# Performance work log

Hardware: AMD Instinct MI355X
Metric: run time of the kernel (lower is better)

## Reference

```python
import jax, jax.numpy as jnp
import numpy as np

BEV = 128          # bev_res
EMBED = 128        # embed_dim
HEADS = 8
POINTS = 4
HD = EMBED // HEADS  # head dim = 16


def setup_inputs() -> dict:
    key = jax.random.key(0)
    ks = jax.random.split(key, 9)
    bs, nq = 4, BEV * BEV
    s = lambda k, shape: jax.random.normal(k, shape, jnp.float32) * 0.02
    return {
        "query": jax.random.normal(ks[0], (bs, nq, EMBED), jnp.float32),
        "W_off": s(ks[1], (EMBED, HEADS * POINTS * 2)),
        "b_off": s(ks[2], (HEADS * POINTS * 2,)),
        "W_attn": s(ks[3], (EMBED, HEADS * POINTS)),
        "b_attn": s(ks[4], (HEADS * POINTS,)),
        "W_val": s(ks[5], (EMBED, EMBED)),
        "b_val": s(ks[6], (EMBED,)),
        "W_out": s(ks[7], (EMBED, EMBED)),
        "b_out": s(ks[8], (EMBED,)),
    }


def _ref_points():
    # matches np.meshgrid(linspace(0,1,BEV), linspace(0,1,BEV), indexing='ij');
    # stacked as (col, row) = (x, y), flattened row-major to (BEV*BEV, 2)
    lin = jnp.linspace(0.0, 1.0, BEV)
    gy, gx = jnp.meshgrid(lin, lin, indexing="ij")
    return jnp.stack([gx, gy], axis=-1).reshape(-1, 2)


def _msda(query, W_off, b_off, W_attn, b_attn, W_val, b_val, W_out, b_out):
    bs, nq, _ = query.shape
    H = W = BEV
    # value projection; single level so num_value == nq == H*W
    value = query @ W_val + b_val
    v = value.reshape(bs, nq, HEADS, HD).transpose(0, 2, 1, 3)  # (bs, heads, HW, hd)

    # sampling offsets and attention weights (softmax over levels*points = points)
    off = (query @ W_off + b_off).reshape(bs, nq, HEADS, POINTS, 2)
    aw = jax.nn.softmax((query @ W_attn + b_attn).reshape(bs, nq, HEADS, POINTS), axis=-1)

    ref = _ref_points()  # (nq, 2) in [0,1], (x, y)
    norm = jnp.array([W, H], jnp.float32)  # offset_normalizer = (W, H)
    loc = ref[None, :, None, None, :] + off / norm  # (bs, nq, heads, pts, 2)

    # grid_sample bilinear, align_corners=False, padding_mode='zeros'
    px = loc[..., 0] * W - 0.5
    py = loc[..., 1] * H - 0.5
    x0 = jnp.floor(px)
    y0 = jnp.floor(py)
    wx = px - x0  # weight toward x0+1
    wy = py - y0
    x0i = x0.astype(jnp.int32)
    y0i = y0.astype(jnp.int32)

    def flat(a):  # (bs, nq, heads, pts) -> (bs, heads, nq*pts)
        return a.transpose(0, 2, 1, 3).reshape(bs, HEADS, nq * POINTS)

    def samp(xi, yi):
        valid = ((xi >= 0) & (xi < W) & (yi >= 0) & (yi < H)).astype(v.dtype)
        xc = jnp.clip(xi, 0, W - 1)
        yc = jnp.clip(yi, 0, H - 1)
        idx = flat(yc * W + xc)  # (bs, heads, nq*pts)
        g = jnp.take_along_axis(v, idx[..., None], axis=2)  # (bs, heads, nq*pts, hd)
        return g * flat(valid)[..., None]

    s00 = samp(x0i, y0i)
    s01 = samp(x0i + 1, y0i)
    s10 = samp(x0i, y0i + 1)
    s11 = samp(x0i + 1, y0i + 1)
    wxf = flat(wx)[..., None]
    wyf = flat(wy)[..., None]
    sampled = (s00 * (1 - wxf) * (1 - wyf) + s01 * wxf * (1 - wyf)
               + s10 * (1 - wxf) * wyf + s11 * wxf * wyf)
    sampled = sampled.reshape(bs, HEADS, nq, POINTS, HD)

    awt = aw.transpose(0, 2, 1, 3)  # (bs, heads, nq, pts)
    out = jnp.einsum("bhnpd,bhnp->bnhd", sampled, awt).reshape(bs, nq, EMBED)
    out = out @ W_out + b_out
    # mmcv MSDA adds identity (=query) internally; SelfAttention adds residual again
    return out + 2.0 * query


def reference(query, W_off, b_off, W_attn, b_attn, W_val, b_val, W_out, b_out):
    return _msda(query, W_off, b_off, W_attn, b_attn, W_val, b_val, W_out, b_out)
```

## Files before the change

### kernel.cpp

```cpp
#include <hip/hip_runtime.h>

#define BS 4
#define NQ 16384

typedef unsigned short u16;
typedef unsigned int u32;
typedef unsigned char u8;
typedef __attribute__((ext_vector_type(8))) short bf16x8;
typedef __attribute__((ext_vector_type(4))) short bf16x4;
typedef __attribute__((ext_vector_type(4))) float f32x4;
typedef __attribute__((ext_vector_type(2))) float f32x2;

__device__ __forceinline__ float bf2f(u16 v) { return __uint_as_float(((u32)v) << 16); }
__device__ __forceinline__ u16 f2bf(float f) {
    u32 u = __float_as_uint(f);
    return (u16)((u + 0x7fffu + ((u >> 16) & 1u)) >> 16);
}
__device__ __forceinline__ u32 pk_trunc(float lo, float hi) {
    return __builtin_amdgcn_perm(__float_as_uint(hi), __float_as_uint(lo), 0x07060302u);
}

union ABu { bf16x8 v; u32 u[4]; };

__global__ __launch_bounds__(256)
void setup_kernel(const float* __restrict__ W_val, const float* __restrict__ W_off,
                  const float* __restrict__ W_attn, const float* __restrict__ W_out,
                  u16* __restrict__ Wswz, u16* __restrict__ Wout_swz)
{
    const int i = blockIdx.x * 256 + threadIdx.x;
    if (i < 28672) {
        const int j = i & 7, lane = (i >> 3) & 15, quad = (i >> 7) & 3;
        const int kb = (i >> 9) & 3, nt = i >> 11;
        const int k = kb * 32 + quad * 8 + j;
        const int n = nt * 16 + lane;
        float v;
        if (n < 128)      v = W_val[k * 128 + n];
        else if (n < 192) v = W_off[k * 64 + (n - 128)];
        else              v = W_attn[k * 32 + (n - 192)];
        Wswz[i] = f2bf(v);
    } else if (i < 45056) {
        const int i2 = i - 28672;
        const int j = i2 & 7, lane = (i2 >> 3) & 15, quad = (i2 >> 7) & 3;
        const int kb = (i2 >> 9) & 3, nt = i2 >> 11;
        const int k = kb * 32 + quad * 8 + j;
        const int n = nt * 16 + lane;
        Wout_swz[i2] = f2bf(W_out[k * 128 + n]);
    }
}

__global__ __launch_bounds__(256, 4)
void fused_kernel(const float* __restrict__ query,
                  const float* __restrict__ b_off, const float* __restrict__ b_attn,
                  const float* __restrict__ b_val, const float* __restrict__ b_out,
                  const u16* __restrict__ Wswz, const u16* __restrict__ Wout_swz,
                  float* __restrict__ out)
{
    __shared__ __align__(16) u8  vhalo[144 * 144];
    __shared__ __align__(16) u16 scratch[64 * 136];

    const int tid = threadIdx.x;
    const int bid = blockIdx.x;
    const int b_  = bid >> 8;
    const int sq  = bid & 255;
    const int Y   = (sq >> 4) * 8;
    const int X   = (sq & 15) * 8;

    const int w = tid >> 6, l = tid & 63;
    const int lane16 = l & 15, quad = l >> 4;
    const size_t batch_base = (size_t)b_ * NQ;

    const bf16x8* Wf  = (const bf16x8*)Wswz;
    const bf16x8* WfO = (const bf16x8*)Wout_swz;

    {
        const int tl = w * 16 + lane16;
        const int ty = tl >> 3, tx = tl & 7;
        const float* qrow = query + (batch_base + (size_t)(Y + ty) * 128 + (X + tx)) * 128
                          + quad * 8;
        bf16x8 qfrag[4];
        #pragma unroll
        for (int kb = 0; kb < 4; ++kb) {
            f32x4 q0 = *(const f32x4*)(qrow + kb * 32);
            f32x4 q1 = *(const f32x4*)(qrow + kb * 32 + 4);
            ABu ab;
            ab.u[0] = pk_trunc(q0.x, q0.y); ab.u[1] = pk_trunc(q0.z, q0.w);
            ab.u[2] = pk_trunc(q1.x, q1.y); ab.u[3] = pk_trunc(q1.z, q1.w);
            qfrag[kb] = ab.v;
        }
        #pragma unroll
        for (int ntile = 0; ntile < 6; ++ntile) {
            const int nt = 8 + ntile;
            f32x4 acc = {0.f, 0.f, 0.f, 0.f};
            const bf16x8* wp = Wf + ((size_t)(nt * 4) * 4 + quad) * 16 + lane16;
            #pragma unroll
            for (int kb = 0; kb < 4; ++kb)
                acc = __builtin_amdgcn_mfma_f32_16x16x32_bf16(wp[kb * 64], qfrag[kb], acc, 0, 0, 0);
            const int c = ntile * 16 + quad * 4;
            const float4 bias = (ntile < 4) ? *(const float4*)&b_off[c]
                                            : *(const float4*)&b_attn[c - 64];
            uint2 pk;
            pk.x = pk_trunc(acc[0] + bias.x, acc[1] + bias.y);
            pk.y = pk_trunc(acc[2] + bias.z, acc[3] + bias.w);
            *(uint2*)&scratch[tl * 96 + c] = pk;
        }
    }

    #pragma unroll
    for (int i = 0; i < 3; ++i) {
        const int a = w + 4 * i;
        if (a >= 9) break;
        const int hp = a * 16 + lane16;
        const int hy = hp / 12, hx = hp - hy * 12;
        const int gy = min(max(Y - 2 + hy, 0), 127);
        const int gx = min(max(X - 2 + hx, 0), 127);
        const float* qrow = query + (batch_base + (size_t)gy * 128 + gx) * 128 + quad * 8;
        bf16x8 qfrag[4];
        #pragma unroll
        for (int kb = 0; kb < 4; ++kb) {
            f32x4 q0 = *(const f32x4*)(qrow + kb * 32);
            f32x4 q1 = *(const f32x4*)(qrow + kb * 32 + 4);
            ABu ab;
            ab.u[0] = pk_trunc(q0.x, q0.y); ab.u[1] = pk_trunc(q0.z, q0.w);
            ab.u[2] = pk_trunc(q1.x, q1.y); ab.u[3] = pk_trunc(q1.z, q1.w);
            qfrag[kb] = ab.v;
        }
        #pragma unroll
        for (int mt = 0; mt < 8; ++mt) {
            f32x4 acc = {0.f, 0.f, 0.f, 0.f};
            const bf16x8* wp = Wf + ((size_t)(mt * 4) * 4 + quad) * 16 + lane16;
            #pragma unroll
            for (int kb = 0; kb < 4; ++kb)
                acc = __builtin_amdgcn_mfma_f32_16x16x32_bf16(wp[kb * 64], qfrag[kb], acc, 0, 0, 0);
            const int d0 = mt * 16 + quad * 4;
            const float4 bias = *(const float4*)&b_val[d0];
            u32 pk = __builtin_amdgcn_cvt_pk_fp8_f32(acc[0] + bias.x, acc[1] + bias.y, 0, false);
            pk     = __builtin_amdgcn_cvt_pk_fp8_f32(acc[2] + bias.z, acc[3] + bias.w, pk, true);
            *(u32*)&vhalo[hp * 144 + d0] = pk;
        }
    }
    __syncthreads();

    float aw[2][4], ox[2][4], oy[2][4];
    #pragma unroll
    for (int it = 0; it < 2; ++it) {
        const int item = it * 256 + tid;
        const int t = item >> 3, h = item & 7;
        bf16x8 ofr = *(const bf16x8*)&scratch[t * 96 + h * 8];
        bf16x4 atr = *(const bf16x4*)&scratch[t * 96 + 64 + h * 4];
        #pragma unroll
        for (int p = 0; p < 4; ++p) {
            ox[it][p] = bf2f((u16)ofr[2 * p]);
            oy[it][p] = bf2f((u16)ofr[2 * p + 1]);
        }
        const float l0 = bf2f((u16)atr[0]), l1 = bf2f((u16)atr[1]);
        const float l2 = bf2f((u16)atr[2]), l3 = bf2f((u16)atr[3]);
        const float m = fmaxf(fmaxf(l0, l1), fmaxf(l2, l3));
        const float e0 = __expf(l0 - m), e1 = __expf(l1 - m);
        const float e2 = __expf(l2 - m), e3 = __expf(l3 - m);
        const float inv = 1.0f / (e0 + e1 + e2 + e3);
        aw[it][0] = e0 * inv; aw[it][1] = e1 * inv;
        aw[it][2] = e2 * inv; aw[it][3] = e3 * inv;
    }
    __syncthreads();

    #pragma unroll
    for (int it = 0; it < 2; ++it) {
        const int item = it * 256 + tid;
        const int t = item >> 3, h = item & 7;
        const int qx = X + (t & 7), qy = Y + (t >> 3);
        const float cx = (float)qx * (128.0f / 127.0f);
        const float cy = (float)qy * (128.0f / 127.0f);

        f32x2 acc2[8];
        #pragma unroll
        for (int d = 0; d < 8; ++d) acc2[d] = (f32x2){0.f, 0.f};

        #pragma unroll
        for (int p = 0; p < 4; ++p) {
            const float px = cx + ox[it][p] - 0.5f;
            const float py = cy + oy[it][p] - 0.5f;
            const float fx = floorf(px), fy = floorf(py);
            const float wx = px - fx, wy = py - fy;
            const int xi = (int)fx, yi = (int)fy;
            const float cw[4] = {(1.f - wx) * (1.f - wy), wx * (1.f - wy),
                                 (1.f - wx) * wy,         wx * wy};
            const int hx0 = min(max(xi - X + 2, 0), 11), hx1 = min(hx0 + 1, 11);
            const int hy0 = min(max(yi - Y + 2, 0), 11), hy1 = min(hy0 + 1, 11);
            const int cxs[4] = {hx0, hx1, hx0, hx1};
            const int cys[4] = {hy0, hy0, hy1, hy1};
            const int gxs[4] = {xi, xi + 1, xi, xi + 1};
            const int gys[4] = {yi, yi, yi + 1, yi + 1};
            #pragma unroll
            for (int c4 = 0; c4 < 4; ++c4) {
                const bool valid = (gxs[c4] >= 0) & (gxs[c4] < 128) &
                                   (gys[c4] >= 0) & (gys[c4] < 128);
                const float wgt = valid ? cw[c4] * aw[it][p] : 0.f;
                const f32x2 w2 = {wgt, wgt};
                const int hp = cys[c4] * 12 + cxs[c4];
                const int4 rv = *(const int4*)&vhalo[hp * 144 + h * 16];
                acc2[0] += w2 * __builtin_amdgcn_cvt_pk_f32_fp8(rv.x, false);
                acc2[1] += w2 * __builtin_amdgcn_cvt_pk_f32_fp8(rv.x, true);
                acc2[2] += w2 * __builtin_amdgcn_cvt_pk_f32_fp8(rv.y, false);
                acc2[3] += w2 * __builtin_amdgcn_cvt_pk_f32_fp8(rv.y, true);
                acc2[4] += w2 * __builtin_amdgcn_cvt_pk_f32_fp8(rv.z, false);
                acc2[5] += w2 * __builtin_amdgcn_cvt_pk_f32_fp8(rv.z, true);
                acc2[6] += w2 * __builtin_amdgcn_cvt_pk_f32_fp8(rv.w, false);
                acc2[7] += w2 * __builtin_amdgcn_cvt_pk_f32_fp8(rv.w, true);
            }
        }
        uint4 s0, s1;
        s0.x = pk_trunc(acc2[0][0], acc2[0][1]); s0.y = pk_trunc(acc2[1][0], acc2[1][1]);
        s0.z = pk_trunc(acc2[2][0], acc2[2][1]); s0.w = pk_trunc(acc2[3][0], acc2[3][1]);
        s1.x = pk_trunc(acc2[4][0], acc2[4][1]); s1.y = pk_trunc(acc2[5][0], acc2[5][1]);
        s1.z = pk_trunc(acc2[6][0], acc2[6][1]); s1.w = pk_trunc(acc2[7][0], acc2[7][1]);
        *(uint4*)&scratch[t * 136 + h * 16]     = s0;
        *(uint4*)&scratch[t * 136 + h * 16 + 8] = s1;
    }
    __syncthreads();

    {
        bf16x8 afrag[4];
        #pragma unroll
        for (int kb = 0; kb < 4; ++kb)
            afrag[kb] = *(const bf16x8*)&scratch[(w * 16 + lane16) * 136 + kb * 32 + quad * 8];

        #pragma unroll
        for (int nt = 0; nt < 8; ++nt) {
            f32x4 acc = {0.f, 0.f, 0.f, 0.f};
            const bf16x8* bp = WfO + ((size_t)(nt * 4) * 4 + quad) * 16 + lane16;
            #pragma unroll
            for (int kb = 0; kb < 4; ++kb)
                acc = __builtin_amdgcn_mfma_f32_16x16x32_bf16(afrag[kb], bp[kb * 64], acc, 0, 0, 0);
            const int n = nt * 16 + lane16;
            const float bias = b_out[n];
            #pragma unroll
            for (int r = 0; r < 4; ++r) {
                const int tl = w * 16 + quad * 4 + r;
                const size_t grow = batch_base + (size_t)(Y + (tl >> 3)) * 128 + (X + (tl & 7));
                const float q = query[grow * 128 + n];
                out[grow * 128 + n] = acc[r] + bias + 2.0f * q;
            }
        }
    }
}

extern "C" void kernel_launch(void* const* d_in, const int* in_sizes, int n_in,
                              void* d_out, int out_size, void* d_ws, size_t ws_size,
                              hipStream_t stream)
{
    const float* query  = (const float*)d_in[0];
    const float* W_off  = (const float*)d_in[1];
    const float* b_off  = (const float*)d_in[2];
    const float* W_attn = (const float*)d_in[3];
    const float* b_attn = (const float*)d_in[4];
    const float* W_val  = (const float*)d_in[5];
    const float* b_val  = (const float*)d_in[6];
    const float* W_out  = (const float*)d_in[7];
    const float* b_out  = (const float*)d_in[8];
    float* out = (float*)d_out;

    u16* Wswz     = (u16*)d_ws;
    u16* Wout_swz = (u16*)((char*)d_ws + 28672 * 2);

    setup_kernel<<<176, 256, 0, stream>>>(W_val, W_off, W_attn, W_out, Wswz, Wout_swz);
    fused_kernel<<<1024, 256, 0, stream>>>(query, b_off, b_attn, b_val, b_out,
                                           Wswz, Wout_swz, out);
}
```

Measured before the change: 140.1 us.

## Batch query loads up front, remap blocks per XCD, prefetch residual, nontemporal stores

Blocks are remapped so that each XCD handles a contiguous band of one batch image, which is meant to improve L2 reuse of the overlapping halo rows. All query loads for the own tile and the halo tiles are now issued together before the MFMA work, so their memory latency overlaps with compute. The residual query values are prefetched into registers before the sampling phase, and output writes use nontemporal stores. Occupancy is lowered from 4 to 3 blocks per SM to make room for the extra registers, which risks hiding less latency.

```diff
diff --git a/kernel.cpp b/kernel.cpp
--- a/kernel.cpp
+++ b/kernel.cpp
@@ -21,6 +21,25 @@
 }
 
 union ABu { bf16x8 v; u32 u[4]; };
+
+__device__ __forceinline__ void load8(f32x4* buf, const float* p) {
+    #pragma unroll
+    for (int kb = 0; kb < 4; ++kb) {
+        buf[2 * kb]     = *(const f32x4*)(p + kb * 32);
+        buf[2 * kb + 1] = *(const f32x4*)(p + kb * 32 + 4);
+    }
+}
+__device__ __forceinline__ void cvt_frag(const f32x4* buf, bf16x8* frag) {
+    #pragma unroll
+    for (int kb = 0; kb < 4; ++kb) {
+        ABu ab;
+        ab.u[0] = pk_trunc(buf[2 * kb].x,     buf[2 * kb].y);
+        ab.u[1] = pk_trunc(buf[2 * kb].z,     buf[2 * kb].w);
+        ab.u[2] = pk_trunc(buf[2 * kb + 1].x, buf[2 * kb + 1].y);
+        ab.u[3] = pk_trunc(buf[2 * kb + 1].z, buf[2 * kb + 1].w);
+        frag[kb] = ab.v;
+    }
+}
 
 __global__ __launch_bounds__(256)
 void setup_kernel(const float* __restrict__ W_val, const float* __restrict__ W_off,
@@ -48,7 +67,7 @@
     }
 }
 
-__global__ __launch_bounds__(256, 4)
+__global__ __launch_bounds__(256, 3)
 void fused_kernel(const float* __restrict__ query,
                   const float* __restrict__ b_off, const float* __restrict__ b_attn,
                   const float* __restrict__ b_val, const float* __restrict__ b_out,
@@ -60,10 +79,11 @@
 
     const int tid = threadIdx.x;
     const int bid = blockIdx.x;
-    const int b_  = bid >> 8;
-    const int sq  = bid & 255;
-    const int Y   = (sq >> 4) * 8;
-    const int X   = (sq & 15) * 8;
+    const int xcd = bid & 7;
+    const int ii  = bid >> 3;
+    const int b_  = xcd >> 1;
+    const int Y   = (((xcd & 1) << 3) | (ii >> 4)) << 3;
+    const int X   = (ii & 15) << 3;
 
     const int w = tid >> 6, l = tid & 63;
     const int lane16 = l & 15, quad = l >> 4;
@@ -74,19 +94,38 @@
 
     {
         const int tl = w * 16 + lane16;
-        const int ty = tl >> 3, tx = tl & 7;
-        const float* qrow = query + (batch_base + (size_t)(Y + ty) * 128 + (X + tx)) * 128
-                          + quad * 8;
-        bf16x8 qfrag[4];
-        #pragma unroll
-        for (int kb = 0; kb < 4; ++kb) {
-            f32x4 q0 = *(const f32x4*)(qrow + kb * 32);
-            f32x4 q1 = *(const f32x4*)(qrow + kb * 32 + 4);
-            ABu ab;
-            ab.u[0] = pk_trunc(q0.x, q0.y); ab.u[1] = pk_trunc(q0.z, q0.w);
-            ab.u[2] = pk_trunc(q1.x, q1.y); ab.u[3] = pk_trunc(q1.z, q1.w);
-            qfrag[kb] = ab.v;
-        }
+        const float* qp_own = query +
+            (batch_base + (size_t)(Y + (tl >> 3)) * 128 + (X + (tl & 7))) * 128 + quad * 8;
+
+        const int a1 = w, a2 = 4 + w;
+        const float* qp1;
+        const float* qp2;
+        const float* qp3;
+        {
+            int hp = a1 * 16 + lane16;
+            int hy = hp / 12, hx = hp - hy * 12;
+            qp1 = query + (batch_base +
+                  (size_t)min(max(Y - 2 + hy, 0), 127) * 128 +
+                  min(max(X - 2 + hx, 0), 127)) * 128 + quad * 8;
+            hp = a2 * 16 + lane16;
+            hy = hp / 12; hx = hp - hy * 12;
+            qp2 = query + (batch_base +
+                  (size_t)min(max(Y - 2 + hy, 0), 127) * 128 +
+                  min(max(X - 2 + hx, 0), 127)) * 128 + quad * 8;
+            hp = 8 * 16 + lane16;
+            hy = hp / 12; hx = hp - hy * 12;
+            qp3 = query + (batch_base +
+                  (size_t)min(max(Y - 2 + hy, 0), 127) * 128 +
+                  min(max(X - 2 + hx, 0), 127)) * 128 + quad * 8;
+        }
+
+        f32x4 A[8], B[8], C[8], D[8];
+        load8(A, qp_own);
+        load8(B, qp1);
+        load8(C, qp2);
+
+        bf16x8 qf[4];
+        cvt_frag(A, qf);
         #pragma unroll
         for (int ntile = 0; ntile < 6; ++ntile) {
             const int nt = 8 + ntile;
@@ -94,7 +133,7 @@
             const bf16x8* wp = Wf + ((size_t)(nt * 4) * 4 + quad) * 16 + lane16;
             #pragma unroll
             for (int kb = 0; kb < 4; ++kb)
-                acc = __builtin_amdgcn_mfma_f32_16x16x32_bf16(wp[kb * 64], qfrag[kb], acc, 0, 0, 0);
+                acc = __builtin_amdgcn_mfma_f32_16x16x32_bf16(wp[kb * 64], qf[kb], acc, 0, 0, 0);
             const int c = ntile * 16 + quad * 4;
             const float4 bias = (ntile < 4) ? *(const float4*)&b_off[c]
                                             : *(const float4*)&b_attn[c - 64];
@@ -103,39 +142,42 @@
             pk.y = pk_trunc(acc[2] + bias.z, acc[3] + bias.w);
             *(uint2*)&scratch[tl * 96 + c] = pk;
         }
-    }
-
-    #pragma unroll
-    for (int i = 0; i < 3; ++i) {
-        const int a = w + 4 * i;
-        if (a >= 9) break;
-        const int hp = a * 16 + lane16;
-        const int hy = hp / 12, hx = hp - hy * 12;
-        const int gy = min(max(Y - 2 + hy, 0), 127);
-        const int gx = min(max(X - 2 + hx, 0), 127);
-        const float* qrow = query + (batch_base + (size_t)gy * 128 + gx) * 128 + quad * 8;
-        bf16x8 qfrag[4];
-        #pragma unroll
-        for (int kb = 0; kb < 4; ++kb) {
-            f32x4 q0 = *(const f32x4*)(qrow + kb * 32);
-            f32x4 q1 = *(const f32x4*)(qrow + kb * 32 + 4);
-            ABu ab;
-            ab.u[0] = pk_trunc(q0.x, q0.y); ab.u[1] = pk_trunc(q0.z, q0.w);
-            ab.u[2] = pk_trunc(q1.x, q1.y); ab.u[3] = pk_trunc(q1.z, q1.w);
-            qfrag[kb] = ab.v;
-        }
-        #pragma unroll
-        for (int mt = 0; mt < 8; ++mt) {
-            f32x4 acc = {0.f, 0.f, 0.f, 0.f};
-            const bf16x8* wp = Wf + ((size_t)(mt * 4) * 4 + quad) * 16 + lane16;
-            #pragma unroll
-            for (int kb = 0; kb < 4; ++kb)
-                acc = __builtin_amdgcn_mfma_f32_16x16x32_bf16(wp[kb * 64], qfrag[kb], acc, 0, 0, 0);
-            const int d0 = mt * 16 + quad * 4;
-            const float4 bias = *(const float4*)&b_val[d0];
-            u32 pk = __builtin_amdgcn_cvt_pk_fp8_f32(acc[0] + bias.x, acc[1] + bias.y, 0, false);
-            pk     = __builtin_amdgcn_cvt_pk_fp8_f32(acc[2] + bias.z, acc[3] + bias.w, pk, true);
-            *(u32*)&vhalo[hp * 144 + d0] = pk;
+        if (w == 0) load8(D, qp3);
+
+        #pragma unroll
+        for (int tsel = 0; tsel < 2; ++tsel) {
+            cvt_frag(tsel ? C : B, qf);
+            const int hp = (tsel ? a2 : a1) * 16 + lane16;
+            #pragma unroll
+            for (int mt = 0; mt < 8; ++mt) {
+                f32x4 acc = {0.f, 0.f, 0.f, 0.f};
+                const bf16x8* wp = Wf + ((size_t)(mt * 4) * 4 + quad) * 16 + lane16;
+                #pragma unroll
+                for (int kb = 0; kb < 4; ++kb)
+                    acc = __builtin_amdgcn_mfma_f32_16x16x32_bf16(wp[kb * 64], qf[kb], acc, 0, 0, 0);
+                const int d0 = mt * 16 + quad * 4;
+                const float4 bias = *(const float4*)&b_val[d0];
+                u32 pk = __builtin_amdgcn_cvt_pk_fp8_f32(acc[0] + bias.x, acc[1] + bias.y, 0, false);
+                pk     = __builtin_amdgcn_cvt_pk_fp8_f32(acc[2] + bias.z, acc[3] + bias.w, pk, true);
+                *(u32*)&vhalo[hp * 144 + d0] = pk;
+            }
+        }
+        if (w == 0) {
+            cvt_frag(D, qf);
+            const int hp = 8 * 16 + lane16;
+            #pragma unroll
+            for (int mt = 0; mt < 8; ++mt) {
+                f32x4 acc = {0.f, 0.f, 0.f, 0.f};
+                const bf16x8* wp = Wf + ((size_t)(mt * 4) * 4 + quad) * 16 + lane16;
+                #pragma unroll
+                for (int kb = 0; kb < 4; ++kb)
+                    acc = __builtin_amdgcn_mfma_f32_16x16x32_bf16(wp[kb * 64], qf[kb], acc, 0, 0, 0);
+                const int d0 = mt * 16 + quad * 4;
+                const float4 bias = *(const float4*)&b_val[d0];
+                u32 pk = __builtin_amdgcn_cvt_pk_fp8_f32(acc[0] + bias.x, acc[1] + bias.y, 0, false);
+                pk     = __builtin_amdgcn_cvt_pk_fp8_f32(acc[2] + bias.z, acc[3] + bias.w, pk, true);
+                *(u32*)&vhalo[hp * 144 + d0] = pk;
+            }
         }
     }
     __syncthreads();
@@ -162,6 +204,17 @@
         aw[it][2] = e2 * inv; aw[it][3] = e3 * inv;
     }
     __syncthreads();
+
+    float qpre[8][4];
+    #pragma unroll
+    for (int r = 0; r < 4; ++r) {
+        const int tl = w * 16 + quad * 4 + r;
+        const float* qp = query +
+            (batch_base + (size_t)(Y + (tl >> 3)) * 128 + (X + (tl & 7))) * 128 + lane16;
+        #pragma unroll
+        for (int nt = 0; nt < 8; ++nt)
+            qpre[nt][r] = qp[nt * 16];
+    }
 
     #pragma unroll
     for (int it = 0; it < 2; ++it) {
@@ -237,8 +290,8 @@
             for (int r = 0; r < 4; ++r) {
                 const int tl = w * 16 + quad * 4 + r;
                 const size_t grow = batch_base + (size_t)(Y + (tl >> 3)) * 128 + (X + (tl & 7));
-                const float q = query[grow * 128 + n];
-                out[grow * 128 + n] = acc[r] + bias + 2.0f * q;
+                __builtin_nontemporal_store(acc[r] + bias + 2.0f * qpre[nt][r],
+                                            &out[grow * 128 + n]);
             }
         }
     }
```

Result: no change. 142.8 us (+2.0%).
